# Kernel tuning notes

Measured on AMD Instinct MI355X. Metric: run time of the kernel, lower is better.

Reference implementation:

```python
import jax, jax.numpy as jnp
import numpy as np

C = 64
HW = 21 * 21  # 441
NEIGHBOR_K = 3


def setup_inputs() -> dict:
    key = jax.random.key(0)
    k1, k2, k3, k4 = jax.random.split(key, 4)
    B1, B2 = 32, 25
    x1 = jax.random.normal(k1, (B1, C, 21, 21), dtype=jnp.float32)
    x2 = jax.random.normal(k2, (B2, C, 21, 21), dtype=jnp.float32)
    mask1 = jax.random.uniform(k3, (B1, 21, 21), dtype=jnp.float32)
    mask2 = jax.random.uniform(k4, (B2, 21, 21), dtype=jnp.float32)
    return {"x1": x1, "x2": x2, "mask1": mask1, "mask2": mask2}


def reference(x1, x2, mask1, mask2):
    B1 = x1.shape[0]
    B2 = x2.shape[0]
    q = x1.reshape(B1, C, HW)  # (B1, 64, 441) query descriptors
    s = x2.reshape(B2, C, HW)  # (B2, 64, 441) support descriptors
    # per-descriptor L2 norms over channel dim
    qn = jnp.linalg.norm(q, axis=1)  # (B1, 441)
    sn = jnp.linalg.norm(s, axis=1)  # (B2, 441)
    # cosine similarity between every query descriptor and every support descriptor
    inner = jnp.einsum('aci,bcj->abij', q, s)  # (B1, B2, 441, 441)
    sim = inner / (qn[:, None, :, None] * sn[None, :, None, :])
    # mask out invalid spatial positions on both sides
    sim = sim * mask1.reshape(B1, 1, HW, 1) * mask2.reshape(1, B2, 1, HW)
    # top-k nearest support descriptors per query descriptor, sum over all
    topk_vals, _ = jax.lax.top_k(sim, NEIGHBOR_K)  # (B1, B2, 441, k)
    return topk_vals.reshape(B1, B2, -1).sum(axis=2)  # (B1, B2)
```

## Files before the change

kernel.cpp:

```cpp
#include <hip/hip_runtime.h>
#include <math.h>

#define CCH 64
#define HW 441
#define HWP 448
#define NT 28
#define NB2 25
#define PANEL (HWP * CCH)
#define NI 4

typedef _Float16 half8 __attribute__((ext_vector_type(8)));
typedef __fp16 h2 __attribute__((ext_vector_type(2)));
typedef float f32x4 __attribute__((ext_vector_type(4)));

__global__ __launch_bounds__(64) void normalize_frag_kernel(
        const float* __restrict__ x1, const float* __restrict__ m1,
        const float* __restrict__ x2, const float* __restrict__ m2,
        _Float16* __restrict__ qh, _Float16* __restrict__ sh,
        float* __restrict__ out, int nout, int n1rows, int nrows) {
    int idx = blockIdx.x * blockDim.x + threadIdx.x;
    if (idx < nout) out[idx] = 0.f;
    if (idx >= nrows) return;
    const float* x; const float* mk; _Float16* outp; int rb;
    if (idx < n1rows) { x = x1; mk = m1; outp = qh; rb = idx; }
    else             { x = x2; mk = m2; outp = sh; rb = idx - n1rows; }
    int b = rb / HWP, i = rb - b * HWP;
    float vals[CCH];
    if (i < HW) {
        const float* xb = x + (size_t)b * CCH * HW + i;
        float ss = 0.f;
#pragma unroll
        for (int c = 0; c < CCH; ++c) { float v = xb[c * HW]; vals[c] = v; ss += v * v; }
        float scale = mk[b * HW + i] * rsqrtf(ss);
#pragma unroll
        for (int c = 0; c < CCH; ++c) vals[c] *= scale;
    } else {
#pragma unroll
        for (int c = 0; c < CCH; ++c) vals[c] = 0.f;
    }
    _Float16* pb = outp + (size_t)b * PANEL + (i >> 4) * 1024 + (i & 15) * 8;
#pragma unroll
    for (int f = 0; f < 2; ++f) {
#pragma unroll
        for (int qd = 0; qd < 4; ++qd) {
            half8 h;
#pragma unroll
            for (int e = 0; e < 8; ++e) h[e] = (_Float16)vals[f * 32 + qd * 8 + e];
            *(half8*)(pb + f * 512 + qd * 128) = h;
        }
    }
}

static __device__ __forceinline__ h2 hmax2(h2 a, h2 b) {
    return __builtin_elementwise_max(a, b);
}
static __device__ __forceinline__ h2 hmin2(h2 a, h2 b) {
    return __builtin_elementwise_min(a, b);
}

#define PK_INSERT(v, p0, p1, p2)           \
    do {                                   \
        h2 _m = hmax2(p0, v);              \
        h2 _c = hmin2(p0, v);              \
        p0 = _m;                           \
        _m = hmax2(p1, _c);                \
        _c = hmin2(p1, _c);                \
        p1 = _m;                           \
        p2 = hmax2(p2, _c);                \
    } while (0)

#define MERGE3(t0, t1, t2, b0, b1, b2)            \
    do {                                          \
        float _m0 = fmaxf(t0, b0);                \
        float _n0 = fminf(t0, b0);                \
        float _m1 = fmaxf(t1, b1);                \
        float _t2 = fmaxf(t2, b2);                \
        t0 = _m0;                                 \
        t1 = fmaxf(_n0, _m1);                     \
        t2 = fmaxf(fminf(_n0, _m1), _t2);         \
    } while (0)

template <bool MASK>
__device__ __forceinline__ void tile_compute(half8 a0, half8 a1,
                                             const half8 (&bf0)[NI], const half8 (&bf1)[NI],
                                             h2 (&p0)[NI], h2 (&p1)[NI], h2 (&p2)[NI],
                                             int quad) {
    const f32x4 FZ = {0.f, 0.f, 0.f, 0.f};
    const float NEG = -1e30f;
#pragma unroll
    for (int t = 0; t < NI; ++t) {
        f32x4 z = __builtin_amdgcn_mfma_f32_16x16x32_f16(a0, bf0[t], FZ, 0, 0, 0);
        z = __builtin_amdgcn_mfma_f32_16x16x32_f16(a1, bf1[t], z, 0, 0, 0);
        if (MASK) {
#pragma unroll
            for (int r = 0; r < 4; ++r)
                if (quad * 4 + r >= 9) z[r] = NEG;
        }
        h2 c02 = __builtin_amdgcn_cvt_pkrtz(z[0], z[2]);
        h2 c13 = __builtin_amdgcn_cvt_pkrtz(z[1], z[3]);
        PK_INSERT(c02, p0[t], p1[t], p2[t]);
        PK_INSERT(c13, p0[t], p1[t], p2[t]);
    }
}

template <bool MASKED>
__device__ __forceinline__ void do_sweep(const _Float16* __restrict__ qtiles,
                                         const _Float16* __restrict__ spanel,
                                         int jt0, int lane, int quad,
                                         float (&t0)[NI], float (&t1)[NI], float (&t2)[NI]) {
    const h2 NEGH = {(__fp16)-65504.f, (__fp16)-65504.f};
    half8 bf0[NI], bf1[NI];
#pragma unroll
    for (int t = 0; t < NI; ++t) {
        const _Float16* qp = qtiles + t * 1024 + lane * 8;
        bf0[t] = *(const half8*)qp;
        bf1[t] = *(const half8*)(qp + 512);
    }
    h2 p0[NI], p1[NI], p2[NI];
#pragma unroll
    for (int t = 0; t < NI; ++t) { p0[t] = NEGH; p1[t] = NEGH; p2[t] = NEGH; }

    const _Float16* sp = spanel + (size_t)jt0 * 1024 + lane * 8;
    half8 c0a = *(const half8*)(sp);
    half8 c0b = *(const half8*)(sp + 512);
    half8 c1a = *(const half8*)(sp + 1024);
    half8 c1b = *(const half8*)(sp + 1024 + 512);
    half8 n0a = *(const half8*)(sp + 2048);
    half8 n0b = *(const half8*)(sp + 2048 + 512);
    half8 n1a = *(const half8*)(sp + 3072);
    half8 n1b = *(const half8*)(sp + 3072 + 512);

    for (int it = 0; it < 6; ++it) {
        int pf0 = 2 * it + 4; if (pf0 > 13) pf0 = 13;
        int pf1 = 2 * it + 5; if (pf1 > 13) pf1 = 13;
        const _Float16* pp0 = sp + (size_t)pf0 * 1024;
        const _Float16* pp1 = sp + (size_t)pf1 * 1024;
        half8 f0a = *(const half8*)pp0;
        half8 f0b = *(const half8*)(pp0 + 512);
        half8 f1a = *(const half8*)pp1;
        half8 f1b = *(const half8*)(pp1 + 512);

        tile_compute<false>(c0a, c0b, bf0, bf1, p0, p1, p2, quad);
        tile_compute<false>(c1a, c1b, bf0, bf1, p0, p1, p2, quad);

        c0a = n0a; c0b = n0b; c1a = n1a; c1b = n1b;
        n0a = f0a; n0b = f0b; n1a = f1a; n1b = f1b;
    }
    tile_compute<false>(c0a, c0b, bf0, bf1, p0, p1, p2, quad);
    tile_compute<MASKED>(c1a, c1b, bf0, bf1, p0, p1, p2, quad);

#pragma unroll
    for (int t = 0; t < NI; ++t) {
        float a0 = (float)p0[t][0], a1 = (float)p1[t][0], a2 = (float)p2[t][0];
        float b0 = (float)p0[t][1], b1 = (float)p1[t][1], b2 = (float)p2[t][1];
        MERGE3(a0, a1, a2, b0, b1, b2);
        b0 = __shfl_xor(a0, 16); b1 = __shfl_xor(a1, 16); b2 = __shfl_xor(a2, 16);
        MERGE3(a0, a1, a2, b0, b1, b2);
        b0 = __shfl_xor(a0, 32); b1 = __shfl_xor(a1, 32); b2 = __shfl_xor(a2, 32);
        MERGE3(a0, a1, a2, b0, b1, b2);
        t0[t] = a0; t1[t] = a1; t2[t] = a2;
    }
}

__global__ __launch_bounds__(128) void sim_topk_mfma(const _Float16* __restrict__ qh,
                                                     const _Float16* __restrict__ sh,
                                                     float* __restrict__ out) {
    __shared__ float s_tri[2][NI][16][3];
    int blk = blockIdx.x;
    int pair = blk / 7, g = blk - pair * 7;
    int a = pair / NB2, b = pair - a * NB2;
    int tid = threadIdx.x, wave = tid >> 6, lane = tid & 63;
    int m = lane & 15, quad = lane >> 4;
    const _Float16* qtiles = qh + (size_t)a * PANEL + (size_t)g * NI * 1024;
    const _Float16* spanel = sh + (size_t)b * PANEL;

    float t0[NI], t1[NI], t2[NI];
    if (wave == 0)
        do_sweep<false>(qtiles, spanel, 0, lane, quad, t0, t1, t2);
    else
        do_sweep<true>(qtiles, spanel, 14, lane, quad, t0, t1, t2);

    if (quad == 0) {
#pragma unroll
        for (int t = 0; t < NI; ++t) {
            s_tri[wave][t][m][0] = t0[t];
            s_tri[wave][t][m][1] = t1[t];
            s_tri[wave][t][m][2] = t2[t];
        }
    }
    __syncthreads();

    if (wave == 0) {
        int t = quad;
        float a0 = s_tri[0][t][m][0], a1 = s_tri[0][t][m][1], a2 = s_tri[0][t][m][2];
        float b0 = s_tri[1][t][m][0], b1 = s_tri[1][t][m][1], b2 = s_tri[1][t][m][2];
        MERGE3(a0, a1, a2, b0, b1, b2);
        float r = a0 + a1 + a2;
#pragma unroll
        for (int off = 32; off > 0; off >>= 1) r += __shfl_down(r, off);
        if (lane == 0) atomicAdd(&out[pair], r);
    }
}

extern "C" void kernel_launch(void* const* d_in, const int* in_sizes, int n_in,
                              void* d_out, int out_size, void* d_ws, size_t ws_size,
                              hipStream_t stream) {
    const float* x1 = (const float*)d_in[0];
    const float* x2 = (const float*)d_in[1];
    const float* m1 = (const float*)d_in[2];
    const float* m2 = (const float*)d_in[3];
    float* out = (float*)d_out;

    int B1 = in_sizes[0] / (CCH * HW);
    int B2 = in_sizes[1] / (CCH * HW);

    _Float16* qh = (_Float16*)d_ws;
    _Float16* sh = qh + (size_t)B1 * PANEL;

    int n1 = B1 * HWP, ntot = (B1 + B2) * HWP;
    normalize_frag_kernel<<<(ntot + 63) / 64, 64, 0, stream>>>(
        x1, m1, x2, m2, qh, sh, out, B1 * B2, n1, ntot);
    sim_topk_mfma<<<B1 * B2 * 7, 128, 0, stream>>>(qh, sh, out);
}
```

Before: 100.5 us.

## Stage support panel in LDS and share across eight waves per pair

Each block now handles a whole (query, support) pair with 8 waves, 4 query groups of 7 tiles each times 2 support halves. The support panel is copied once into shared memory and reused by all waves, instead of each of 7 small blocks reloading it from global memory with register prefetch. The aim is to cut redundant global/L2 traffic for the support panel. In exchange, NI=7 raises register pressure, the block needs about 56KB of LDS, and the software prefetch is replaced by plain LDS loads.

```diff
diff --git a/kernel.cpp b/kernel.cpp
--- a/kernel.cpp
+++ b/kernel.cpp
@@ -7,7 +7,7 @@
 #define NT 28
 #define NB2 25
 #define PANEL (HWP * CCH)
-#define NI 4
+#define NI 7
 
 typedef _Float16 half8 __attribute__((ext_vector_type(8)));
 typedef __fp16 h2 __attribute__((ext_vector_type(2)));
@@ -103,51 +103,55 @@
     }
 }
 
-template <bool MASKED>
-__device__ __forceinline__ void do_sweep(const _Float16* __restrict__ qtiles,
-                                         const _Float16* __restrict__ spanel,
-                                         int jt0, int lane, int quad,
-                                         float (&t0)[NI], float (&t1)[NI], float (&t2)[NI]) {
-    const h2 NEGH = {(__fp16)-65504.f, (__fp16)-65504.f};
+__global__ __launch_bounds__(512, 4) void sim_topk_mfma(const _Float16* __restrict__ qh,
+                                                        const _Float16* __restrict__ sh,
+                                                        float* __restrict__ out) {
+    __shared__ _Float16 s_panel[NT * 1024];
+    __shared__ float s_tri[4][2][NI][16][3];
+
+    int pair = blockIdx.x;
+    int a = pair / NB2, b = pair - a * NB2;
+    int tid = threadIdx.x, wave = tid >> 6, lane = tid & 63;
+    int m = lane & 15, quad = lane >> 4;
+    int ig = wave >> 1, jhalf = wave & 1;
+
+    const _Float16* qbase = qh + (size_t)a * PANEL + (size_t)ig * NI * 1024;
     half8 bf0[NI], bf1[NI];
 #pragma unroll
     for (int t = 0; t < NI; ++t) {
-        const _Float16* qp = qtiles + t * 1024 + lane * 8;
+        const _Float16* qp = qbase + t * 1024 + lane * 8;
         bf0[t] = *(const half8*)qp;
         bf1[t] = *(const half8*)(qp + 512);
     }
+
+    {
+        const float4* src = (const float4*)(sh + (size_t)b * PANEL);
+        float4* dst = (float4*)s_panel;
+#pragma unroll
+        for (int it = 0; it < 7; ++it)
+            dst[it * 512 + tid] = src[it * 512 + tid];
+    }
+    __syncthreads();
+
+    const h2 NEGH = {(__fp16)-65504.f, (__fp16)-65504.f};
     h2 p0[NI], p1[NI], p2[NI];
 #pragma unroll
     for (int t = 0; t < NI; ++t) { p0[t] = NEGH; p1[t] = NEGH; p2[t] = NEGH; }
 
-    const _Float16* sp = spanel + (size_t)jt0 * 1024 + lane * 8;
-    half8 c0a = *(const half8*)(sp);
-    half8 c0b = *(const half8*)(sp + 512);
-    half8 c1a = *(const half8*)(sp + 1024);
-    half8 c1b = *(const half8*)(sp + 1024 + 512);
-    half8 n0a = *(const half8*)(sp + 2048);
-    half8 n0b = *(const half8*)(sp + 2048 + 512);
-    half8 n1a = *(const half8*)(sp + 3072);
-    half8 n1b = *(const half8*)(sp + 3072 + 512);
-
-    for (int it = 0; it < 6; ++it) {
-        int pf0 = 2 * it + 4; if (pf0 > 13) pf0 = 13;
-        int pf1 = 2 * it + 5; if (pf1 > 13) pf1 = 13;
-        const _Float16* pp0 = sp + (size_t)pf0 * 1024;
-        const _Float16* pp1 = sp + (size_t)pf1 * 1024;
-        half8 f0a = *(const half8*)pp0;
-        half8 f0b = *(const half8*)(pp0 + 512);
-        half8 f1a = *(const half8*)pp1;
-        half8 f1b = *(const half8*)(pp1 + 512);
-
-        tile_compute<false>(c0a, c0b, bf0, bf1, p0, p1, p2, quad);
-        tile_compute<false>(c1a, c1b, bf0, bf1, p0, p1, p2, quad);
-
-        c0a = n0a; c0b = n0b; c1a = n1a; c1b = n1b;
-        n0a = f0a; n0b = f0b; n1a = f1a; n1b = f1b;
-    }
-    tile_compute<false>(c0a, c0b, bf0, bf1, p0, p1, p2, quad);
-    tile_compute<MASKED>(c1a, c1b, bf0, bf1, p0, p1, p2, quad);
+    const _Float16* sp = s_panel + jhalf * 14 * 1024 + lane * 8;
+    for (int jt = 0; jt < 13; ++jt) {
+        half8 a0 = *(const half8*)(sp + jt * 1024);
+        half8 a1 = *(const half8*)(sp + jt * 1024 + 512);
+        tile_compute<false>(a0, a1, bf0, bf1, p0, p1, p2, quad);
+    }
+    {
+        half8 a0 = *(const half8*)(sp + 13 * 1024);
+        half8 a1 = *(const half8*)(sp + 13 * 1024 + 512);
+        if (jhalf)
+            tile_compute<true>(a0, a1, bf0, bf1, p0, p1, p2, quad);
+        else
+            tile_compute<false>(a0, a1, bf0, bf1, p0, p1, p2, quad);
+    }
 
 #pragma unroll
     for (int t = 0; t < NI; ++t) {
@@ -158,48 +162,26 @@
         MERGE3(a0, a1, a2, b0, b1, b2);
         b0 = __shfl_xor(a0, 32); b1 = __shfl_xor(a1, 32); b2 = __shfl_xor(a2, 32);
         MERGE3(a0, a1, a2, b0, b1, b2);
-        t0[t] = a0; t1[t] = a1; t2[t] = a2;
-    }
-}
-
-__global__ __launch_bounds__(128) void sim_topk_mfma(const _Float16* __restrict__ qh,
-                                                     const _Float16* __restrict__ sh,
-                                                     float* __restrict__ out) {
-    __shared__ float s_tri[2][NI][16][3];
-    int blk = blockIdx.x;
-    int pair = blk / 7, g = blk - pair * 7;
-    int a = pair / NB2, b = pair - a * NB2;
-    int tid = threadIdx.x, wave = tid >> 6, lane = tid & 63;
-    int m = lane & 15, quad = lane >> 4;
-    const _Float16* qtiles = qh + (size_t)a * PANEL + (size_t)g * NI * 1024;
-    const _Float16* spanel = sh + (size_t)b * PANEL;
-
-    float t0[NI], t1[NI], t2[NI];
-    if (wave == 0)
-        do_sweep<false>(qtiles, spanel, 0, lane, quad, t0, t1, t2);
-    else
-        do_sweep<true>(qtiles, spanel, 14, lane, quad, t0, t1, t2);
-
-    if (quad == 0) {
-#pragma unroll
-        for (int t = 0; t < NI; ++t) {
-            s_tri[wave][t][m][0] = t0[t];
-            s_tri[wave][t][m][1] = t1[t];
-            s_tri[wave][t][m][2] = t2[t];
+        if (quad == 0) {
+            s_tri[ig][jhalf][t][m][0] = a0;
+            s_tri[ig][jhalf][t][m][1] = a1;
+            s_tri[ig][jhalf][t][m][2] = a2;
         }
     }
     __syncthreads();
 
-    if (wave == 0) {
-        int t = quad;
-        float a0 = s_tri[0][t][m][0], a1 = s_tri[0][t][m][1], a2 = s_tri[0][t][m][2];
-        float b0 = s_tri[1][t][m][0], b1 = s_tri[1][t][m][1], b2 = s_tri[1][t][m][2];
-        MERGE3(a0, a1, a2, b0, b1, b2);
-        float r = a0 + a1 + a2;
-#pragma unroll
-        for (int off = 32; off > 0; off >>= 1) r += __shfl_down(r, off);
-        if (lane == 0) atomicAdd(&out[pair], r);
-    }
+    float r = 0.f;
+    if (tid < 448) {
+        int pi = tid / 112, c = tid - pi * 112;
+        int t = c >> 4, mm = c & 15;
+        float a0 = s_tri[pi][0][t][mm][0], a1 = s_tri[pi][0][t][mm][1], a2 = s_tri[pi][0][t][mm][2];
+        float b0 = s_tri[pi][1][t][mm][0], b1 = s_tri[pi][1][t][mm][1], b2 = s_tri[pi][1][t][mm][2];
+        MERGE3(a0, a1, a2, b0, b1, b2);
+        r = a0 + a1 + a2;
+    }
+#pragma unroll
+    for (int off = 32; off > 0; off >>= 1) r += __shfl_down(r, off);
+    if (lane == 0) atomicAdd(&out[pair], r);
 }
 
 extern "C" void kernel_launch(void* const* d_in, const int* in_sizes, int n_in,
@@ -220,5 +202,5 @@
     int n1 = B1 * HWP, ntot = (B1 + B2) * HWP;
     normalize_frag_kernel<<<(ntot + 63) / 64, 64, 0, stream>>>(
         x1, m1, x2, m2, qh, sh, out, B1 * B2, n1, ntot);
-    sim_topk_mfma<<<B1 * B2 * 7, 128, 0, stream>>>(qh, sh, out);
-}
+    sim_topk_mfma<<<B1 * B2, 512, 0, stream>>>(qh, sh, out);
+}
```

Result: slower. 102.9 us (+2.3%).
